# Performance work log

Hardware: AMD Instinct MI355X
Metric: run time of the kernel (lower is better)

Reference implementation:

```python
import jax, jax.numpy as jnp
import numpy as np

KS = 3
K3 = KS ** 3
NUM_K = 4
KM_ITERS = 10  # fixed Lloyd iterations (original runs to tolerance)


def _unfold3d(xp, d, h, w):
    # xp: [B, C, d+2, h+2, w+2] -> [B, C, d, h, w, 27]; kernel dims flattened as (k1,k2,k3)
    sl = [xp[:, :, i:i + d, j:j + h, l:l + w]
          for i in range(KS) for j in range(KS) for l in range(KS)]
    return jnp.stack(sl, axis=-1)


def _kmeans(pts):
    # pts: [N, C]. Deterministic init with first NUM_K points, fixed Lloyd iterations.
    cent0 = pts[:NUM_K]

    def assign(cent):
        d2 = (jnp.sum(pts * pts, -1, keepdims=True)
              - 2.0 * (pts @ cent.T) + jnp.sum(cent * cent, -1))  # [N, K]
        return jnp.argmin(d2, axis=-1)

    def step(cent, _):
        oh = jax.nn.one_hot(assign(cent), NUM_K, dtype=pts.dtype)  # [N, K]
        cnt = jnp.maximum(oh.sum(0), 1.0)
        cent = (oh.T @ pts) / cnt[:, None]
        return cent, None

    cent, _ = jax.lax.scan(step, cent0, None, length=KM_ITERS)
    return assign(cent), cent


def _mlp3(z, w1, b1, w2, b2, w3, b3):
    z = jax.nn.relu(z @ w1 + b1)
    z = jax.nn.relu(z @ w2 + b2)
    return z @ w3 + b3


def reference(x, proj_w, base_w, gk_w1, gk_b1, gk_w2, gk_b2, gk_w3, gk_b3,
              gb_w1, gb_b1, gb_w2, gb_b2, gb_w3, gb_b3, prelu_a):
    b, c, d, h, w = x.shape
    o = base_w.shape[0]
    n = d * h * w
    x_in = x
    # 1x1x1 input projection (no bias)
    xp = jnp.einsum('oi,bidhw->bodhw', proj_w, x)
    xp = jnp.pad(xp, ((0, 0), (0, 0), (1, 1), (1, 1), (1, 1)))
    patches = _unfold3d(xp, d, h, w)                                # [b,c,d,h,w,27]
    # mean_type 's': mean over kernel dims -> per-voxel channel summary
    x_mean = patches.mean(-1).reshape(b, c, n).transpose(0, 2, 1)   # [b,n,c]
    idx, cent = jax.vmap(_kmeans)(x_mean)                           # [b,n], [b,K,c]
    feat = cent.reshape(b, NUM_K * c)
    # per-cluster dynamic kernel gates in (0,1)
    w_i = jax.nn.sigmoid(_mlp3(feat, gk_w1, gk_b1, gk_w2, gk_b2, gk_w3, gk_b3))
    w_i = w_i.reshape(b, NUM_K, K3).transpose(1, 0, 2)[:, :, None, None, :]  # [K,b,1,1,27]
    weight = (w_i * base_w).reshape(NUM_K, b, o, c * K3)            # [K,b,o,c*27]
    bias = _mlp3(feat, gb_w1, gb_b1, gb_w2, gb_b2, gb_w3, gb_b3)
    bias = bias.reshape(b, NUM_K, o).transpose(1, 0, 2)[..., None]  # [K,b,o,1]
    # im2col: [b, c*27, n] with (c, k) channel-major flattening as in the torch rearrange
    xf = patches.reshape(b, c, n, K3).transpose(0, 1, 3, 2).reshape(b, c * K3, n)
    out = jnp.einsum('kbof,bfn->kbon', weight, xf) + bias           # [K,b,o,n]
    mask = jax.nn.one_hot(idx, NUM_K, dtype=out.dtype)              # [b,n,K]
    out = (out * mask.transpose(2, 0, 1)[:, :, None, :]).sum(0)     # [b,o,n]
    out = out.reshape(b, o, d, h, w)
    out = jnp.where(out >= 0, out, prelu_a * out)                   # PReLU (single param)
    return out + x_in


def setup_inputs():
    key = jax.random.key(0)
    ks = jax.random.split(key, 12)
    B, C, O, D = 1, 64, 64, 40
    inner, inner2 = 128, 64
    fin = C * NUM_K

    def lin(k, i, o_):
        s = 1.0 / np.sqrt(i)
        return jax.random.uniform(k, (i, o_), jnp.float32, -s, s)

    return {
        'x': jax.random.normal(ks[0], (B, C, D, D, D), jnp.float32),
        'proj_w': jax.random.normal(ks[1], (C, C), jnp.float32) / np.sqrt(C),
        'base_w': jax.random.normal(ks[2], (O, C, K3), jnp.float32) / np.sqrt(C * K3),
        'gk_w1': lin(ks[3], fin, inner), 'gk_b1': jnp.zeros((inner,), jnp.float32),
        'gk_w2': lin(ks[4], inner, inner), 'gk_b2': jnp.zeros((inner,), jnp.float32),
        'gk_w3': lin(ks[5], inner, K3 * NUM_K), 'gk_b3': jnp.zeros((K3 * NUM_K,), jnp.float32),
        'gb_w1': lin(ks[6], fin, inner2), 'gb_b1': jnp.zeros((inner2,), jnp.float32),
        'gb_w2': lin(ks[7], inner2, inner2), 'gb_b2': jnp.zeros((inner2,), jnp.float32),
        'gb_w3': lin(ks[8], inner2, O * NUM_K), 'gb_b3': jnp.zeros((O * NUM_K,), jnp.float32),
        'prelu_a': jnp.full((1,), 0.25, jnp.float32),
    }
```

## Files before the change

kernel.cpp:

```cpp
#include <hip/hip_runtime.h>
#include <math.h>

typedef short v8s __attribute__((ext_vector_type(8)));
typedef float v4f __attribute__((ext_vector_type(4)));

#define NVOX 64000
#define NPAD 74088
#define P2   1764
#define GSTR 592704
#define NCPY 32
#define ITST (NCPY*260)

__device__ __forceinline__ unsigned short bf16rne(float f){
  unsigned int u = __float_as_uint(f);
  u += 0x7FFFu + ((u >> 16) & 1u);
  return (unsigned short)(u >> 16);
}

__global__ __launch_bounds__(256) void prep_k(const float* __restrict__ x,
                                              const float* __restrict__ pw,
                                              float* __restrict__ xp,
                                              short* __restrict__ xpt,
                                              const float* __restrict__ bw,
                                              short* __restrict__ bwb,
                                              float* __restrict__ km){
  int tid = threadIdx.x;
  int bid = blockIdx.x;
  if (bid < 1000){
    int m = (bid >> 2) * 256 + tid;
    int quarter = bid & 3;
    float xv[64];
#pragma unroll
    for (int i = 0; i < 64; i++) xv[i] = x[(size_t)i * NVOX + m];
    int d = m / 1600; int r = m - d * 1600; int h = r / 40; int w = r - h * 40;
    int p = ((d + 1) * 42 + (h + 1)) * 42 + (w + 1);
    const float4* pw4 = (const float4*)pw;
    for (int g8 = quarter * 2; g8 < quarter * 2 + 2; g8++){
      v8s pk;
#pragma unroll
      for (int j = 0; j < 8; j++){
        int co = g8 * 8 + j;
        float acc = 0.f;
#pragma unroll
        for (int q = 0; q < 16; q++){
          float4 pv = pw4[co * 16 + q];
          acc = fmaf(pv.x, xv[4*q+0], acc);
          acc = fmaf(pv.y, xv[4*q+1], acc);
          acc = fmaf(pv.z, xv[4*q+2], acc);
          acc = fmaf(pv.w, xv[4*q+3], acc);
        }
        xp[(size_t)co * NVOX + m] = acc;
        pk[j] = (short)bf16rne(acc);
      }
      *(v8s*)(xpt + (size_t)g8 * GSTR + (size_t)p * 8) = pk;
    }
  } else if (bid < 1432){
    int e = (bid - 1000) * 256 + tid;
    int t5 = e >> 12; int rem = e & 4095;
    int o = rem >> 6; int c = rem & 63;
    bwb[e] = (short)bf16rne(bw[(o * 64 + c) * 27 + t5]);
  } else if (bid < 1472){
    v8s z = (v8s){0,0,0,0,0,0,0,0};
    for (int p = (bid - 1432) * 256 + tid; p < NPAD; p += 40 * 256){
      int d = p / P2; int rem = p - d * P2; int h = rem / 42; int w = rem - h * 42;
      if (d == 0 || d == 41 || h == 0 || h == 41 || w == 0 || w == 41){
#pragma unroll
        for (int g = 0; g < 8; g++)
          *(v8s*)(xpt + (size_t)g * GSTR + (size_t)p * 8) = z;
      }
    }
  } else {
    for (int j = (bid - 1472) * 256 + tid; j < 10 * ITST; j += 82 * 256)
      km[j] = 0.f;
  }
}

__global__ __launch_bounds__(256) void boxwh_k(const float* __restrict__ in,
                                               float* __restrict__ out){
  __shared__ float s0[1600], s1[1600];
  size_t base = (size_t)blockIdx.x * 1600;
  int t = threadIdx.x;
  for (int e = t; e < 1600; e += 256) s0[e] = in[base + e];
  __syncthreads();
  for (int e = t; e < 1600; e += 256){
    int w = e % 40;
    float s = s0[e];
    if (w > 0)  s += s0[e - 1];
    if (w < 39) s += s0[e + 1];
    s1[e] = s;
  }
  __syncthreads();
  for (int e = t; e < 1600; e += 256){
    int h = e / 40;
    float s = s1[e];
    if (h > 0)  s += s1[e - 40];
    if (h < 39) s += s1[e + 40];
    out[base + e] = s;
  }
}

__global__ __launch_bounds__(256) void boxdt_k(const float* __restrict__ in,
                                               float* __restrict__ out,
                                               float* __restrict__ acc1){
  __shared__ float tile[64][65];
  __shared__ float s_cent[256];
  __shared__ float s_cc[4];
  __shared__ float s_red[260];
  __shared__ int   s_kb[64];
  int t = threadIdx.x;
  int nb = blockIdx.x * 64;
  int l = t & 63, g = t >> 6;
  {
    int k = t >> 6, c = t & 63;
    s_cent[t] = (in[(size_t)c * NVOX + k] + in[(size_t)c * NVOX + k + 1600]) * (1.f / 27.f);
  }
  for (int j = t; j < 260; j += 256) s_red[j] = 0.f;
  int n = nb + l;
  int d = n / 1600;
  for (int cc = g; cc < 64; cc += 4){
    const float* b = in + (size_t)cc * NVOX + n;
    float s = b[0];
    if (d > 0)  s += b[-1600];
    if (d < 39) s += b[1600];
    tile[cc][l] = s * (1.f / 27.f);
  }
  __syncthreads();
  if (t < 4){
    float s = 0.f;
    for (int c = 0; c < 64; c++){ float v = s_cent[t * 64 + c]; s = fmaf(v, v, s); }
    s_cc[t] = s;
  }
  __syncthreads();
  if (t < 64){
    float d0 = 0.f, d1 = 0.f, d2 = 0.f, d3 = 0.f;
    for (int c = 0; c < 64; c++){
      float v = tile[c][t];
      d0 = fmaf(s_cent[c], v, d0);
      d1 = fmaf(s_cent[64 + c], v, d1);
      d2 = fmaf(s_cent[128 + c], v, d2);
      d3 = fmaf(s_cent[192 + c], v, d3);
    }
    float sc0 = s_cc[0] - 2.f * d0;
    float sc1 = s_cc[1] - 2.f * d1;
    float sc2 = s_cc[2] - 2.f * d2;
    float sc3 = s_cc[3] - 2.f * d3;
    int kb = 0; float bs = sc0;
    if (sc1 < bs){ bs = sc1; kb = 1; }
    if (sc2 < bs){ bs = sc2; kb = 2; }
    if (sc3 < bs){ bs = sc3; kb = 3; }
    s_kb[t] = kb;
  }
  __syncthreads();
  {
    int lane = t & 63, wv = t >> 6;
    float a0 = 0.f, a1 = 0.f, a2 = 0.f, a3 = 0.f;
#pragma unroll
    for (int j = 0; j < 16; j++){
      int p = wv * 16 + j;
      float v = tile[lane][p];
      int kj = s_kb[p];
      a0 += (kj == 0) ? v : 0.f;
      a1 += (kj == 1) ? v : 0.f;
      a2 += (kj == 2) ? v : 0.f;
      a3 += (kj == 3) ? v : 0.f;
    }
    atomicAdd(&s_red[lane], a0);
    atomicAdd(&s_red[64 + lane], a1);
    atomicAdd(&s_red[128 + lane], a2);
    atomicAdd(&s_red[192 + lane], a3);
  }
  if (t < 4){
    float c = 0.f;
    for (int p = 0; p < 64; p++) c += (s_kb[p] == t) ? 1.f : 0.f;
    s_red[256 + t] = c;
  }
  __syncthreads();
  float* kslot = acc1 + (blockIdx.x & (NCPY - 1)) * 260;
  for (int j = t; j < 260; j += 256) atomicAdd(&kslot[j], s_red[j]);
  for (int nn = g; nn < 64; nn += 4)
    out[(size_t)(nb + nn) * 64 + l] = tile[l][nn];
}

__global__ __launch_bounds__(256) void assign_k(const float* __restrict__ xmt,
                                                const float* __restrict__ kin,
                                                float* __restrict__ kout){
  __shared__ float s_cent[256];
  __shared__ float s_cc[4];
  __shared__ float s_red[260];
  __shared__ float s_x[256 * 65];
  __shared__ int   s_kb[256];
  int t = threadIdx.x, lane = t & 63, wv = t >> 6;
  int n = blockIdx.x * 256 + t;
  {
    float sum = 0.f, cnt = 0.f;
#pragma unroll
    for (int s = 0; s < NCPY; s++){
      sum += kin[s * 260 + t];
      cnt += kin[s * 260 + 256 + (t >> 6)];
    }
    s_cent[t] = sum / fmaxf(cnt, 1.f);
  }
  for (int j = t; j < 260; j += 256) s_red[j] = 0.f;
  __syncthreads();
  if (t < 4){
    const float4* cc4 = (const float4*)(s_cent + t * 64);
    float s = 0.f;
#pragma unroll
    for (int q = 0; q < 16; q++){
      float4 v = cc4[q];
      s = fmaf(v.x, v.x, s); s = fmaf(v.y, v.y, s);
      s = fmaf(v.z, v.z, s); s = fmaf(v.w, v.w, s);
    }
    s_cc[t] = s;
  }
  __syncthreads();
  const float4* xt = (const float4*)(xmt + (size_t)n * 64);
  float4 xq[16];
#pragma unroll
  for (int q = 0; q < 16; q++) xq[q] = xt[q];
  float d0 = 0.f, d1 = 0.f, d2 = 0.f, d3 = 0.f;
  const float4* c4 = (const float4*)s_cent;
#pragma unroll
  for (int q = 0; q < 16; q++){
    float4 p0 = c4[q], p1 = c4[16 + q], p2 = c4[32 + q], p3 = c4[48 + q];
    d0 = fmaf(p0.x, xq[q].x, d0); d0 = fmaf(p0.y, xq[q].y, d0);
    d0 = fmaf(p0.z, xq[q].z, d0); d0 = fmaf(p0.w, xq[q].w, d0);
    d1 = fmaf(p1.x, xq[q].x, d1); d1 = fmaf(p1.y, xq[q].y, d1);
    d1 = fmaf(p1.z, xq[q].z, d1); d1 = fmaf(p1.w, xq[q].w, d1);
    d2 = fmaf(p2.x, xq[q].x, d2); d2 = fmaf(p2.y, xq[q].y, d2);
    d2 = fmaf(p2.z, xq[q].z, d2); d2 = fmaf(p2.w, xq[q].w, d2);
    d3 = fmaf(p3.x, xq[q].x, d3); d3 = fmaf(p3.y, xq[q].y, d3);
    d3 = fmaf(p3.z, xq[q].z, d3); d3 = fmaf(p3.w, xq[q].w, d3);
  }
  float sc0 = s_cc[0] - 2.f * d0;
  float sc1 = s_cc[1] - 2.f * d1;
  float sc2 = s_cc[2] - 2.f * d2;
  float sc3 = s_cc[3] - 2.f * d3;
  int kb = 0; float bs = sc0;
  if (sc1 < bs){ bs = sc1; kb = 1; }
  if (sc2 < bs){ bs = sc2; kb = 2; }
  if (sc3 < bs){ bs = sc3; kb = 3; }
  s_kb[t] = kb;
#pragma unroll
  for (int q = 0; q < 16; q++){
    s_x[t * 65 + 4*q + 0] = xq[q].x;
    s_x[t * 65 + 4*q + 1] = xq[q].y;
    s_x[t * 65 + 4*q + 2] = xq[q].z;
    s_x[t * 65 + 4*q + 3] = xq[q].w;
  }
  __syncthreads();
  float a0 = 0.f, a1 = 0.f, a2 = 0.f, a3 = 0.f;
  int rowbase = wv * 64;
#pragma unroll 16
  for (int j = 0; j < 64; j++){
    float v = s_x[(rowbase + j) * 65 + lane];
    int kj = s_kb[rowbase + j];
    a0 += (kj == 0) ? v : 0.f;
    a1 += (kj == 1) ? v : 0.f;
    a2 += (kj == 2) ? v : 0.f;
    a3 += (kj == 3) ? v : 0.f;
  }
  atomicAdd(&s_red[lane], a0);
  atomicAdd(&s_red[64 + lane], a1);
  atomicAdd(&s_red[128 + lane], a2);
  atomicAdd(&s_red[192 + lane], a3);
#pragma unroll
  for (int kk = 0; kk < 4; kk++){
    unsigned long long m = __ballot(kb == kk);
    if (lane == 0) atomicAdd(&s_red[256 + kk], (float)__popcll(m));
  }
  __syncthreads();
  float* kslot = kout + (blockIdx.x & (NCPY - 1)) * 260;
  for (int j = t; j < 260; j += 256) atomicAdd(&kslot[j], s_red[j]);
}

__global__ __launch_bounds__(256) void conv_k(const short* __restrict__ xpt,
                                              const short* __restrict__ bwb,
                                              const float* __restrict__ km,
                                              const float* __restrict__ xmt,
                                              const float* __restrict__ x,
                                              const float* __restrict__ pa,
                                              float* __restrict__ out,
                      const float* __restrict__ w1, const float* __restrict__ b1,
                      const float* __restrict__ w2, const float* __restrict__ b2,
                      const float* __restrict__ w3, const float* __restrict__ b3,
                      const float* __restrict__ u1, const float* __restrict__ c1,
                      const float* __restrict__ u2, const float* __restrict__ c2,
                      const float* __restrict__ u3, const float* __restrict__ c3){
  static const int POFF[27] = {
    -P2-42-1, -P2-42, -P2-42+1, -P2-1, -P2, -P2+1, -P2+42-1, -P2+42, -P2+42+1,
    -42-1, -42, -42+1, -1, 0, 1, 42-1, 42, 42+1,
    P2-42-1, P2-42, P2-42+1, P2-1, P2, P2+1, P2+42-1, P2+42, P2+42+1 };
  __shared__ float s_wi[108];
  __shared__ float s_bias[256];
  __shared__ float s_acc[64 * 68];
  __shared__ float s_cent[256];
  __shared__ float s_cc[4];
  __shared__ int   s_kb[64];
  __shared__ float s_h1[128], s_h2[128], s_g1[64], s_g2[64];
  int tid = threadIdx.x;
  int vb = blockIdx.x * 64;
  {
    float sum = 0.f, cnt = 0.f;
#pragma unroll
    for (int s = 0; s < NCPY; s++){
      sum += km[s * 260 + tid];
      cnt += km[s * 260 + 256 + (tid >> 6)];
    }
    s_cent[tid] = sum / fmaxf(cnt, 1.f);
  }
  {
    const float4* src = (const float4*)(xmt + (size_t)vb * 64);
#pragma unroll
    for (int j = tid; j < 1024; j += 256){
      float4 v = src[j];
      float* dst = s_acc + (j >> 4) * 68 + (j & 15) * 4;
      dst[0] = v.x; dst[1] = v.y; dst[2] = v.z; dst[3] = v.w;
    }
  }
  __syncthreads();
  if (tid < 4){
    const float4* cc4 = (const float4*)(s_cent + tid * 64);
    float s = 0.f;
#pragma unroll
    for (int q = 0; q < 16; q++){
      float4 v = cc4[q];
      s = fmaf(v.x, v.x, s); s = fmaf(v.y, v.y, s);
      s = fmaf(v.z, v.z, s); s = fmaf(v.w, v.w, s);
    }
    s_cc[tid] = s;
  }
  __syncthreads();
  if (tid < 64){
    const float* xr = s_acc + tid * 68;
    float d0 = 0.f, d1 = 0.f, d2 = 0.f, d3 = 0.f;
#pragma unroll 8
    for (int c = 0; c < 64; c++){
      float v = xr[c];
      d0 = fmaf(s_cent[c], v, d0);
      d1 = fmaf(s_cent[64 + c], v, d1);
      d2 = fmaf(s_cent[128 + c], v, d2);
      d3 = fmaf(s_cent[192 + c], v, d3);
    }
    float sc0 = s_cc[0] - 2.f * d0;
    float sc1 = s_cc[1] - 2.f * d1;
    float sc2 = s_cc[2] - 2.f * d2;
    float sc3 = s_cc[3] - 2.f * d3;
    int kb = 0; float bs = sc0;
    if (sc1 < bs){ bs = sc1; kb = 1; }
    if (sc2 < bs){ bs = sc2; kb = 2; }
    if (sc3 < bs){ bs = sc3; kb = 3; }
    s_kb[tid] = kb;
  }
  if (tid < 128){
    float z0 = 0.f, z1 = 0.f, z2 = 0.f, z3 = 0.f;
#pragma unroll 4
    for (int i = 0; i < 256; i += 4){
      z0 = fmaf(s_cent[i + 0], w1[(i + 0) * 128 + tid], z0);
      z1 = fmaf(s_cent[i + 1], w1[(i + 1) * 128 + tid], z1);
      z2 = fmaf(s_cent[i + 2], w1[(i + 2) * 128 + tid], z2);
      z3 = fmaf(s_cent[i + 3], w1[(i + 3) * 128 + tid], z3);
    }
    s_h1[tid] = fmaxf(b1[tid] + ((z0 + z1) + (z2 + z3)), 0.f);
  } else if (tid < 192){
    int t6 = tid - 128;
    float z0 = 0.f, z1 = 0.f, z2 = 0.f, z3 = 0.f;
#pragma unroll 4
    for (int i = 0; i < 256; i += 4){
      z0 = fmaf(s_cent[i + 0], u1[(i + 0) * 64 + t6], z0);
      z1 = fmaf(s_cent[i + 1], u1[(i + 1) * 64 + t6], z1);
      z2 = fmaf(s_cent[i + 2], u1[(i + 2) * 64 + t6], z2);
      z3 = fmaf(s_cent[i + 3], u1[(i + 3) * 64 + t6], z3);
    }
    s_g1[t6] = fmaxf(c1[t6] + ((z0 + z1) + (z2 + z3)), 0.f);
  }
  __syncthreads();
  if (tid < 128){
    float z0 = 0.f, z1 = 0.f, z2 = 0.f, z3 = 0.f;
#pragma unroll 4
    for (int i = 0; i < 128; i += 4){
      z0 = fmaf(s_h1[i + 0], w2[(i + 0) * 128 + tid], z0);
      z1 = fmaf(s_h1[i + 1], w2[(i + 1) * 128 + tid], z1);
      z2 = fmaf(s_h1[i + 2], w2[(i + 2) * 128 + tid], z2);
      z3 = fmaf(s_h1[i + 3], w2[(i + 3) * 128 + tid], z3);
    }
    s_h2[tid] = fmaxf(b2[tid] + ((z0 + z1) + (z2 + z3)), 0.f);
  } else if (tid < 192){
    int t6 = tid - 128;
    float z0 = 0.f, z1 = 0.f, z2 = 0.f, z3 = 0.f;
#pragma unroll 4
    for (int i = 0; i < 64; i += 4){
      z0 = fmaf(s_g1[i + 0], u2[(i + 0) * 64 + t6], z0);
      z1 = fmaf(s_g1[i + 1], u2[(i + 1) * 64 + t6], z1);
      z2 = fmaf(s_g1[i + 2], u2[(i + 2) * 64 + t6], z2);
      z3 = fmaf(s_g1[i + 3], u2[(i + 3) * 64 + t6], z3);
    }
    s_g2[t6] = fmaxf(c2[t6] + ((z0 + z1) + (z2 + z3)), 0.f);
  }
  __syncthreads();
  if (tid < 108){
    float z0 = 0.f, z1 = 0.f, z2 = 0.f, z3 = 0.f;
#pragma unroll 4
    for (int i = 0; i < 128; i += 4){
      z0 = fmaf(s_h2[i + 0], w3[(i + 0) * 108 + tid], z0);
      z1 = fmaf(s_h2[i + 1], w3[(i + 1) * 108 + tid], z1);
      z2 = fmaf(s_h2[i + 2], w3[(i + 2) * 108 + tid], z2);
      z3 = fmaf(s_h2[i + 3], w3[(i + 3) * 108 + tid], z3);
    }
    float z = b3[tid] + ((z0 + z1) + (z2 + z3));
    s_wi[tid] = 1.f / (1.f + expf(-z));
  }
  {
    float z0 = 0.f, z1 = 0.f, z2 = 0.f, z3 = 0.f;
#pragma unroll 4
    for (int i = 0; i < 64; i += 4){
      z0 = fmaf(s_g2[i + 0], u3[(i + 0) * 256 + tid], z0);
      z1 = fmaf(s_g2[i + 1], u3[(i + 1) * 256 + tid], z1);
      z2 = fmaf(s_g2[i + 2], u3[(i + 2) * 256 + tid], z2);
      z3 = fmaf(s_g2[i + 3], u3[(i + 3) * 256 + tid], z3);
    }
    s_bias[tid] = c3[tid] + ((z0 + z1) + (z2 + z3));
  }
  __syncthreads();
  int wv = tid >> 6, lane = tid & 63;
  int kc = wv & 1, mh = wv >> 1;
  int col = lane & 15, kg = lane >> 4;
  int p4[4], ki4[4];
#pragma unroll
  for (int nt = 0; nt < 4; nt++){
    int v = vb + nt * 16 + col;
    ki4[nt] = s_kb[nt * 16 + col];
    int d = v / 1600; int r = v - d * 1600; int h = r / 40; int w = r - h * 40;
    p4[nt] = ((d + 1) * 42 + (h + 1)) * 42 + (w + 1);
  }
  const short* bg = xpt + (size_t)(kc * 4 + kg) * GSTR;
  const short* bp0 = bg + (size_t)p4[0] * 8;
  const short* bp1 = bg + (size_t)p4[1] * 8;
  const short* bp2 = bg + (size_t)p4[2] * 8;
  const short* bp3 = bg + (size_t)p4[3] * 8;
  int ao0 = (mh * 32 + col) * 64 + kc * 32 + kg * 8;
  int ao1 = ao0 + 16 * 64;
  v4f acc[2][4];
#pragma unroll
  for (int m2 = 0; m2 < 2; m2++)
#pragma unroll
    for (int nt = 0; nt < 4; nt++) acc[m2][nt] = (v4f){0.f, 0.f, 0.f, 0.f};
  v4f zero = {0.f, 0.f, 0.f, 0.f};
#pragma unroll 9
  for (int t = 0; t < 27; t++){
    int po8 = POFF[t] * 8;
    v8s a0 = *(const v8s*)(bwb + t * 4096 + ao0);
    v8s a1 = *(const v8s*)(bwb + t * 4096 + ao1);
    v8s b0 = *(const v8s*)(bp0 + po8);
    v8s b1 = *(const v8s*)(bp1 + po8);
    v8s b2 = *(const v8s*)(bp2 + po8);
    v8s b3 = *(const v8s*)(bp3 + po8);
    float wk0 = s_wi[ki4[0] * 27 + t];
    float wk1 = s_wi[ki4[1] * 27 + t];
    float wk2 = s_wi[ki4[2] * 27 + t];
    float wk3 = s_wi[ki4[3] * 27 + t];
    v4f tp;
    tp = __builtin_amdgcn_mfma_f32_16x16x32_bf16(a0, b0, zero, 0, 0, 0); acc[0][0] += tp * wk0;
    tp = __builtin_amdgcn_mfma_f32_16x16x32_bf16(a1, b0, zero, 0, 0, 0); acc[1][0] += tp * wk0;
    tp = __builtin_amdgcn_mfma_f32_16x16x32_bf16(a0, b1, zero, 0, 0, 0); acc[0][1] += tp * wk1;
    tp = __builtin_amdgcn_mfma_f32_16x16x32_bf16(a1, b1, zero, 0, 0, 0); acc[1][1] += tp * wk1;
    tp = __builtin_amdgcn_mfma_f32_16x16x32_bf16(a0, b2, zero, 0, 0, 0); acc[0][2] += tp * wk2;
    tp = __builtin_amdgcn_mfma_f32_16x16x32_bf16(a1, b2, zero, 0, 0, 0); acc[1][2] += tp * wk2;
    tp = __builtin_amdgcn_mfma_f32_16x16x32_bf16(a0, b3, zero, 0, 0, 0); acc[0][3] += tp * wk3;
    tp = __builtin_amdgcn_mfma_f32_16x16x32_bf16(a1, b3, zero, 0, 0, 0); acc[1][3] += tp * wk3;
  }
  __syncthreads();
  if (kc == 1){
#pragma unroll
    for (int m2 = 0; m2 < 2; m2++)
#pragma unroll
      for (int nt = 0; nt < 4; nt++)
        *(v4f*)(&s_acc[(nt * 16 + col) * 68 + mh * 32 + m2 * 16 + kg * 4]) = acc[m2][nt];
  }
  __syncthreads();
  if (kc == 0){
    float pav = pa[0];
#pragma unroll
    for (int m2 = 0; m2 < 2; m2++){
#pragma unroll
      for (int nt = 0; nt < 4; nt++){
        v4f other = *(const v4f*)(&s_acc[(nt * 16 + col) * 68 + mh * 32 + m2 * 16 + kg * 4]);
        v4f sum = acc[m2][nt] + other;
        int n = vb + nt * 16 + col;
#pragma unroll
        for (int r = 0; r < 4; r++){
          int o = mh * 32 + m2 * 16 + kg * 4 + r;
          float val = sum[r] + s_bias[ki4[nt] * 64 + o];
          val = (val >= 0.f) ? val : pav * val;
          size_t off = (size_t)o * NVOX + n;
          out[off] = val + x[off];
        }
      }
    }
  }
}

extern "C" void kernel_launch(void* const* d_in, const int* in_sizes, int n_in,
                              void* d_out, int out_size, void* d_ws, size_t ws_size,
                              hipStream_t stream){
  const float* x    = (const float*)d_in[0];
  const float* pw   = (const float*)d_in[1];
  const float* bw   = (const float*)d_in[2];
  const float* gkw1 = (const float*)d_in[3];
  const float* gkb1 = (const float*)d_in[4];
  const float* gkw2 = (const float*)d_in[5];
  const float* gkb2 = (const float*)d_in[6];
  const float* gkw3 = (const float*)d_in[7];
  const float* gkb3 = (const float*)d_in[8];
  const float* gbw1 = (const float*)d_in[9];
  const float* gbb1 = (const float*)d_in[10];
  const float* gbw2 = (const float*)d_in[11];
  const float* gbb2 = (const float*)d_in[12];
  const float* gbw3 = (const float*)d_in[13];
  const float* gbb3 = (const float*)d_in[14];
  const float* pa   = (const float*)d_in[15];
  float* outp = (float*)d_out;

  float* ws   = (float*)d_ws;
  float* XP   = ws;
  float* BU2  = ws + 4096000;
  short* XPT  = (short*)(ws + 12288000);
  short* BWB  = XPT + (size_t)NPAD * 64;
  float* KM   = (float*)(BWB + 110592);
  float* XMT  = XP;

  prep_k<<<1554, 256, 0, stream>>>(x, pw, XP, XPT, bw, BWB, KM);
  boxwh_k<<<2560, 256, 0, stream>>>(XP, BU2);
  boxdt_k<<<1000, 256, 0, stream>>>(BU2, XMT, KM);
  for (int it = 1; it <= 9; it++)
    assign_k<<<250, 256, 0, stream>>>(XMT, KM + (it - 1) * ITST, KM + it * ITST);
  conv_k<<<1000, 256, 0, stream>>>(XPT, BWB, KM + 9 * ITST, XMT, x, pa, outp,
                                   gkw1, gkb1, gkw2, gkb2, gkw3, gkb3,
                                   gbw1, gbb1, gbw2, gbb2, gbw3, gbb3);
}
```

Before: 304.6 us.

## Split final assignment and gate MLPs out of conv kernel into one-shot kernel

Before, every one of the 1000 conv blocks recomputed the centroid reduction, the final cluster assignment and the two three-layer gate MLPs redundantly. A new fin_k kernel now computes cluster indices for all voxels and runs the MLPs once in block 0, writing gates, bias and indices to workspace. conv_k then only loads these small arrays before the convolution. This adds an extra kernel launch and a global round trip for the indices, in exchange for removing the per-block serial MLP prologue.

```diff
diff --git a/kernel.cpp b/kernel.cpp
--- a/kernel.cpp
+++ b/kernel.cpp
@@ -274,53 +274,33 @@
   for (int j = t; j < 260; j += 256) atomicAdd(&kslot[j], s_red[j]);
 }
 
-__global__ __launch_bounds__(256) void conv_k(const short* __restrict__ xpt,
-                                              const short* __restrict__ bwb,
-                                              const float* __restrict__ km,
-                                              const float* __restrict__ xmt,
-                                              const float* __restrict__ x,
-                                              const float* __restrict__ pa,
-                                              float* __restrict__ out,
+__global__ __launch_bounds__(256) void fin_k(const float* __restrict__ xmt,
+                                             const float* __restrict__ kin,
+                                             int* __restrict__ idx,
                       const float* __restrict__ w1, const float* __restrict__ b1,
                       const float* __restrict__ w2, const float* __restrict__ b2,
                       const float* __restrict__ w3, const float* __restrict__ b3,
                       const float* __restrict__ u1, const float* __restrict__ c1,
                       const float* __restrict__ u2, const float* __restrict__ c2,
-                      const float* __restrict__ u3, const float* __restrict__ c3){
-  static const int POFF[27] = {
-    -P2-42-1, -P2-42, -P2-42+1, -P2-1, -P2, -P2+1, -P2+42-1, -P2+42, -P2+42+1,
-    -42-1, -42, -42+1, -1, 0, 1, 42-1, 42, 42+1,
-    P2-42-1, P2-42, P2-42+1, P2-1, P2, P2+1, P2+42-1, P2+42, P2+42+1 };
-  __shared__ float s_wi[108];
-  __shared__ float s_bias[256];
-  __shared__ float s_acc[64 * 68];
+                      const float* __restrict__ u3, const float* __restrict__ c3,
+                      float* __restrict__ wi, float* __restrict__ bias){
   __shared__ float s_cent[256];
   __shared__ float s_cc[4];
-  __shared__ int   s_kb[64];
   __shared__ float s_h1[128], s_h2[128], s_g1[64], s_g2[64];
-  int tid = threadIdx.x;
-  int vb = blockIdx.x * 64;
+  int t = threadIdx.x;
+  int n = blockIdx.x * 256 + t;
   {
     float sum = 0.f, cnt = 0.f;
 #pragma unroll
     for (int s = 0; s < NCPY; s++){
-      sum += km[s * 260 + tid];
-      cnt += km[s * 260 + 256 + (tid >> 6)];
-    }
-    s_cent[tid] = sum / fmaxf(cnt, 1.f);
-  }
-  {
-    const float4* src = (const float4*)(xmt + (size_t)vb * 64);
-#pragma unroll
-    for (int j = tid; j < 1024; j += 256){
-      float4 v = src[j];
-      float* dst = s_acc + (j >> 4) * 68 + (j & 15) * 4;
-      dst[0] = v.x; dst[1] = v.y; dst[2] = v.z; dst[3] = v.w;
-    }
-  }
-  __syncthreads();
-  if (tid < 4){
-    const float4* cc4 = (const float4*)(s_cent + tid * 64);
+      sum += kin[s * 260 + t];
+      cnt += kin[s * 260 + 256 + (t >> 6)];
+    }
+    s_cent[t] = sum / fmaxf(cnt, 1.f);
+  }
+  __syncthreads();
+  if (t < 4){
+    const float4* cc4 = (const float4*)(s_cent + t * 64);
     float s = 0.f;
 #pragma unroll
     for (int q = 0; q < 16; q++){
@@ -328,19 +308,27 @@
       s = fmaf(v.x, v.x, s); s = fmaf(v.y, v.y, s);
       s = fmaf(v.z, v.z, s); s = fmaf(v.w, v.w, s);
     }
-    s_cc[tid] = s;
-  }
-  __syncthreads();
-  if (tid < 64){
-    const float* xr = s_acc + tid * 68;
+    s_cc[t] = s;
+  }
+  __syncthreads();
+  {
+    const float4* xt = (const float4*)(xmt + (size_t)n * 64);
+    float4 xq[16];
+#pragma unroll
+    for (int q = 0; q < 16; q++) xq[q] = xt[q];
     float d0 = 0.f, d1 = 0.f, d2 = 0.f, d3 = 0.f;
-#pragma unroll 8
-    for (int c = 0; c < 64; c++){
-      float v = xr[c];
-      d0 = fmaf(s_cent[c], v, d0);
-      d1 = fmaf(s_cent[64 + c], v, d1);
-      d2 = fmaf(s_cent[128 + c], v, d2);
-      d3 = fmaf(s_cent[192 + c], v, d3);
+    const float4* c4 = (const float4*)s_cent;
+#pragma unroll
+    for (int q = 0; q < 16; q++){
+      float4 p0 = c4[q], p1 = c4[16 + q], p2 = c4[32 + q], p3 = c4[48 + q];
+      d0 = fmaf(p0.x, xq[q].x, d0); d0 = fmaf(p0.y, xq[q].y, d0);
+      d0 = fmaf(p0.z, xq[q].z, d0); d0 = fmaf(p0.w, xq[q].w, d0);
+      d1 = fmaf(p1.x, xq[q].x, d1); d1 = fmaf(p1.y, xq[q].y, d1);
+      d1 = fmaf(p1.z, xq[q].z, d1); d1 = fmaf(p1.w, xq[q].w, d1);
+      d2 = fmaf(p2.x, xq[q].x, d2); d2 = fmaf(p2.y, xq[q].y, d2);
+      d2 = fmaf(p2.z, xq[q].z, d2); d2 = fmaf(p2.w, xq[q].w, d2);
+      d3 = fmaf(p3.x, xq[q].x, d3); d3 = fmaf(p3.y, xq[q].y, d3);
+      d3 = fmaf(p3.z, xq[q].z, d3); d3 = fmaf(p3.w, xq[q].w, d3);
     }
     float sc0 = s_cc[0] - 2.f * d0;
     float sc1 = s_cc[1] - 2.f * d1;
@@ -350,20 +338,21 @@
     if (sc1 < bs){ bs = sc1; kb = 1; }
     if (sc2 < bs){ bs = sc2; kb = 2; }
     if (sc3 < bs){ bs = sc3; kb = 3; }
-    s_kb[tid] = kb;
-  }
-  if (tid < 128){
+    idx[n] = kb;
+  }
+  if (blockIdx.x != 0) return;
+  if (t < 128){
     float z0 = 0.f, z1 = 0.f, z2 = 0.f, z3 = 0.f;
 #pragma unroll 4
     for (int i = 0; i < 256; i += 4){
-      z0 = fmaf(s_cent[i + 0], w1[(i + 0) * 128 + tid], z0);
-      z1 = fmaf(s_cent[i + 1], w1[(i + 1) * 128 + tid], z1);
-      z2 = fmaf(s_cent[i + 2], w1[(i + 2) * 128 + tid], z2);
-      z3 = fmaf(s_cent[i + 3], w1[(i + 3) * 128 + tid], z3);
-    }
-    s_h1[tid] = fmaxf(b1[tid] + ((z0 + z1) + (z2 + z3)), 0.f);
-  } else if (tid < 192){
-    int t6 = tid - 128;
+      z0 = fmaf(s_cent[i + 0], w1[(i + 0) * 128 + t], z0);
+      z1 = fmaf(s_cent[i + 1], w1[(i + 1) * 128 + t], z1);
+      z2 = fmaf(s_cent[i + 2], w1[(i + 2) * 128 + t], z2);
+      z3 = fmaf(s_cent[i + 3], w1[(i + 3) * 128 + t], z3);
+    }
+    s_h1[t] = fmaxf(b1[t] + ((z0 + z1) + (z2 + z3)), 0.f);
+  } else if (t < 192){
+    int t6 = t - 128;
     float z0 = 0.f, z1 = 0.f, z2 = 0.f, z3 = 0.f;
 #pragma unroll 4
     for (int i = 0; i < 256; i += 4){
@@ -375,18 +364,18 @@
     s_g1[t6] = fmaxf(c1[t6] + ((z0 + z1) + (z2 + z3)), 0.f);
   }
   __syncthreads();
-  if (tid < 128){
+  if (t < 128){
     float z0 = 0.f, z1 = 0.f, z2 = 0.f, z3 = 0.f;
 #pragma unroll 4
     for (int i = 0; i < 128; i += 4){
-      z0 = fmaf(s_h1[i + 0], w2[(i + 0) * 128 + tid], z0);
-      z1 = fmaf(s_h1[i + 1], w2[(i + 1) * 128 + tid], z1);
-      z2 = fmaf(s_h1[i + 2], w2[(i + 2) * 128 + tid], z2);
-      z3 = fmaf(s_h1[i + 3], w2[(i + 3) * 128 + tid], z3);
-    }
-    s_h2[tid] = fmaxf(b2[tid] + ((z0 + z1) + (z2 + z3)), 0.f);
-  } else if (tid < 192){
-    int t6 = tid - 128;
+      z0 = fmaf(s_h1[i + 0], w2[(i + 0) * 128 + t], z0);
+      z1 = fmaf(s_h1[i + 1], w2[(i + 1) * 128 + t], z1);
+      z2 = fmaf(s_h1[i + 2], w2[(i + 2) * 128 + t], z2);
+      z3 = fmaf(s_h1[i + 3], w2[(i + 3) * 128 + t], z3);
+    }
+    s_h2[t] = fmaxf(b2[t] + ((z0 + z1) + (z2 + z3)), 0.f);
+  } else if (t < 192){
+    int t6 = t - 128;
     float z0 = 0.f, z1 = 0.f, z2 = 0.f, z3 = 0.f;
 #pragma unroll 4
     for (int i = 0; i < 64; i += 4){
@@ -398,38 +387,59 @@
     s_g2[t6] = fmaxf(c2[t6] + ((z0 + z1) + (z2 + z3)), 0.f);
   }
   __syncthreads();
-  if (tid < 108){
+  if (t < 108){
     float z0 = 0.f, z1 = 0.f, z2 = 0.f, z3 = 0.f;
 #pragma unroll 4
     for (int i = 0; i < 128; i += 4){
-      z0 = fmaf(s_h2[i + 0], w3[(i + 0) * 108 + tid], z0);
-      z1 = fmaf(s_h2[i + 1], w3[(i + 1) * 108 + tid], z1);
-      z2 = fmaf(s_h2[i + 2], w3[(i + 2) * 108 + tid], z2);
-      z3 = fmaf(s_h2[i + 3], w3[(i + 3) * 108 + tid], z3);
-    }
-    float z = b3[tid] + ((z0 + z1) + (z2 + z3));
-    s_wi[tid] = 1.f / (1.f + expf(-z));
+      z0 = fmaf(s_h2[i + 0], w3[(i + 0) * 108 + t], z0);
+      z1 = fmaf(s_h2[i + 1], w3[(i + 1) * 108 + t], z1);
+      z2 = fmaf(s_h2[i + 2], w3[(i + 2) * 108 + t], z2);
+      z3 = fmaf(s_h2[i + 3], w3[(i + 3) * 108 + t], z3);
+    }
+    float z = b3[t] + ((z0 + z1) + (z2 + z3));
+    wi[t] = 1.f / (1.f + expf(-z));
   }
   {
     float z0 = 0.f, z1 = 0.f, z2 = 0.f, z3 = 0.f;
 #pragma unroll 4
     for (int i = 0; i < 64; i += 4){
-      z0 = fmaf(s_g2[i + 0], u3[(i + 0) * 256 + tid], z0);
-      z1 = fmaf(s_g2[i + 1], u3[(i + 1) * 256 + tid], z1);
-      z2 = fmaf(s_g2[i + 2], u3[(i + 2) * 256 + tid], z2);
-      z3 = fmaf(s_g2[i + 3], u3[(i + 3) * 256 + tid], z3);
-    }
-    s_bias[tid] = c3[tid] + ((z0 + z1) + (z2 + z3));
-  }
+      z0 = fmaf(s_g2[i + 0], u3[(i + 0) * 256 + t], z0);
+      z1 = fmaf(s_g2[i + 1], u3[(i + 1) * 256 + t], z1);
+      z2 = fmaf(s_g2[i + 2], u3[(i + 2) * 256 + t], z2);
+      z3 = fmaf(s_g2[i + 3], u3[(i + 3) * 256 + t], z3);
+    }
+    bias[t] = c3[t] + ((z0 + z1) + (z2 + z3));
+  }
+}
+
+__global__ __launch_bounds__(256) void conv_k(const short* __restrict__ xpt,
+                                              const short* __restrict__ bwb,
+                                              const float* __restrict__ wi,
+                                              const float* __restrict__ bias,
+                                              const int* __restrict__ idx,
+                                              const float* __restrict__ x,
+                                              const float* __restrict__ pa,
+                                              float* __restrict__ out){
+  static const int POFF[27] = {
+    -P2-42-1, -P2-42, -P2-42+1, -P2-1, -P2, -P2+1, -P2+42-1, -P2+42, -P2+42+1,
+    -42-1, -42, -42+1, -1, 0, 1, 42-1, 42, 42+1,
+    P2-42-1, P2-42, P2-42+1, P2-1, P2, P2+1, P2+42-1, P2+42, P2+42+1 };
+  __shared__ float s_wi[108];
+  __shared__ float s_bias[256];
+  __shared__ float s_acc[64 * 68];
+  int tid = threadIdx.x;
+  for (int j = tid; j < 108; j += 256) s_wi[j] = wi[j];
+  s_bias[tid] = bias[tid];
   __syncthreads();
   int wv = tid >> 6, lane = tid & 63;
   int kc = wv & 1, mh = wv >> 1;
   int col = lane & 15, kg = lane >> 4;
+  int vb = blockIdx.x * 64;
   int p4[4], ki4[4];
 #pragma unroll
   for (int nt = 0; nt < 4; nt++){
     int v = vb + nt * 16 + col;
-    ki4[nt] = s_kb[nt * 16 + col];
+    ki4[nt] = idx[v];
     int d = v / 1600; int r = v - d * 1600; int h = r / 40; int w = r - h * 40;
     p4[nt] = ((d + 1) * 42 + (h + 1)) * 42 + (w + 1);
   }
@@ -527,6 +537,9 @@
   short* XPT  = (short*)(ws + 12288000);
   short* BWB  = XPT + (size_t)NPAD * 64;
   float* KM   = (float*)(BWB + 110592);
+  float* WI   = KM + 10 * ITST;
+  float* BIAS = WI + 108;
+  int*   IDX  = (int*)(BIAS + 256);
   float* XMT  = XP;
 
   prep_k<<<1554, 256, 0, stream>>>(x, pw, XP, XPT, bw, BWB, KM);
@@ -534,7 +547,9 @@
   boxdt_k<<<1000, 256, 0, stream>>>(BU2, XMT, KM);
   for (int it = 1; it <= 9; it++)
     assign_k<<<250, 256, 0, stream>>>(XMT, KM + (it - 1) * ITST, KM + it * ITST);
-  conv_k<<<1000, 256, 0, stream>>>(XPT, BWB, KM + 9 * ITST, XMT, x, pa, outp,
-                                   gkw1, gkb1, gkw2, gkb2, gkw3, gkb3,
-                                   gbw1, gbb1, gbw2, gbb2, gbw3, gbb3);
-}
+  fin_k<<<250, 256, 0, stream>>>(XMT, KM + 9 * ITST, IDX,
+                                 gkw1, gkb1, gkw2, gkb2, gkw3, gkb3,
+                                 gbw1, gbb1, gbw2, gbb2, gbw3, gbb3,
+                                 WI, BIAS);
+  conv_k<<<1000, 256, 0, stream>>>(XPT, BWB, WI, BIAS, IDX, x, pa, outp);
+}
```

After: 300.6 us. About the same (-1.3%).
